# Kernel optimization log

Measured on AMD Instinct MI355X. Metric: run time of the kernel, lower is better.

Reference implementation:

```python
import jax, jax.numpy as jnp
import numpy as np

B, L, HID, TRANS = 16384, 512, 768, 128


def setup_inputs() -> dict:
    key = jax.random.key(0)
    ks = jax.random.split(key, 12)
    def lin(k, out_d, in_d):
        kw, kb = jax.random.split(k)
        s = 1.0 / np.sqrt(in_d)
        return (jax.random.uniform(kw, (out_d, in_d), jnp.float32, -s, s),
                jax.random.uniform(kb, (out_d,), jnp.float32, -s, s))
    W_text, b_text = lin(ks[0], TRANS, HID)
    W_label, b_label = lin(ks[1], TRANS, HID)
    W0, b0 = lin(ks[2], TRANS, 2 * TRANS)
    W1, b1 = lin(ks[3], TRANS, TRANS)
    W2, b2 = lin(ks[4], 1, TRANS)
    target = jax.random.randint(ks[5], (B, L), 0, 2, jnp.int32)
    # guarantee every sample has at least one positive label (torch.mean on empty would NaN)
    target = target.at[:, 0].set(1)
    return {
        "text_embed": jax.random.normal(ks[6], (B, HID), jnp.float32),
        "label_embed": jax.random.normal(ks[7], (L, HID), jnp.float32),
        "target": target,
        "perm": jax.random.permutation(ks[8], B).astype(jnp.int32),
        "W_text": W_text, "b_text": b_text,
        "W_label": W_label, "b_label": b_label,
        "W0": W0, "b0": b0, "W1": W1, "b1": b1, "W2": W2, "b2": b2,
    }


def _network(t, l, W_text, b_text, W_label, b_label, W0, b0, W1, b1, W2, b2):
    tt = t @ W_text.T + b_text            # [B, trans]
    ll = l @ W_label.T + b_label          # [B, trans]
    h = jnp.concatenate([tt, ll], axis=1)  # [B, 2*trans]
    h = jax.nn.relu(h @ W0.T + b0)
    h = jax.nn.relu(h @ W1.T + b1)
    return h @ W2.T + b2                  # [B, 1]


def reference(text_embed, label_embed, target, perm,
              W_text, b_text, W_label, b_label, W0, b0, W1, b1, W2, b2):
    # variable-length mean pooling of label embeddings selected by the multi-hot target
    mask = target.astype(text_embed.dtype)                 # [B, L]
    counts = jnp.maximum(mask.sum(axis=1, keepdims=True), 1.0)
    label_feature_y = (mask @ label_embed) / counts        # [B, hid]
    negative_text = text_embed[perm]                       # shuffled negatives
    params = (W_text, b_text, W_label, b_label, W0, b0, W1, b1, W2, b2)
    E_joint = -jnp.mean(jax.nn.softplus(-_network(text_embed, label_feature_y, *params)))
    E_marginal = jnp.mean(jax.nn.softplus(_network(negative_text, label_feature_y, *params)))
    return E_marginal - E_joint
```

## Files before the change

kernel.cpp:

```cpp
#include <hip/hip_runtime.h>
#include <math.h>

#define BATCH 16384
#define LBL   512
#define HID   768
#define TR    128

typedef unsigned long long u64;
typedef unsigned short ushort_t;
typedef __attribute__((ext_vector_type(8))) short short8;
typedef __attribute__((ext_vector_type(4))) float f32x4;

__device__ __forceinline__ ushort_t f2bf(float f){
  unsigned u = __builtin_bit_cast(unsigned, f);
  u += 0x7FFFu + ((u >> 16) & 1u);
  return (ushort_t)(u >> 16);
}
__device__ __forceinline__ float softplusf(float x){
  return fmaxf(x, 0.0f) + log1pf(expf(-fabsf(x)));
}
__device__ __forceinline__ void gload_lds16(const void* g, void* l){
  __builtin_amdgcn_global_load_lds((const __attribute__((address_space(1))) void*)g,
                                   (__attribute__((address_space(3))) void*)l, 16, 0, 0);
}

__global__ __launch_bounds__(256) void k1(
    const float* __restrict__ W0, const float* __restrict__ Wt, const float* __restrict__ Wl,
    const float* __restrict__ bt, const float* __restrict__ bl, const float* __restrict__ b0,
    const float* __restrict__ W1,
    ushort_t* __restrict__ Msw, ushort_t* __restrict__ Qsw, ushort_t* __restrict__ W1B,
    float* __restrict__ KV, float* __restrict__ out){
  __shared__ float sw[TR];
  int bi = blockIdx.x, t = threadIdx.x;
  if (bi < 256){
    int i = bi & 127;
    int isQ = bi >> 7;
    const float* src = isQ ? Wl : Wt;
    ushort_t* dst = isQ ? Qsw : Msw;
    if (t < TR) sw[t] = W0[(size_t)i*256 + isQ*128 + t];
    if (!isQ && t < 128) W1B[i*128 + t] = f2bf(W1[i*128 + t]);
    __syncthreads();
    int c = t;
    float a0 = 0.f, a1 = 0.f, a2 = 0.f;
    #pragma unroll 8
    for (int a = 0; a < 128; a++){
      float w = sw[a];
      const float* r = src + (size_t)a*HID;
      a0 = fmaf(w, r[c], a0);
      a1 = fmaf(w, r[c+256], a1);
      a2 = fmaf(w, r[c+512], a2);
    }
    int c7 = c & 7;
    dst[(((c      )>>3)<<10) + (i<<3) + c7] = f2bf(a0);
    dst[(((c + 256)>>3)<<10) + (i<<3) + c7] = f2bf(a1);
    dst[(((c + 512)>>3)<<10) + (i<<3) + c7] = f2bf(a2);
  } else {
    if (t < TR){
      float s = b0[t];
      const float* r = W0 + (size_t)t*256;
      for (int a = 0; a < 128; a++) s = fmaf(r[a], bt[a], s);
      for (int a = 0; a < 128; a++) s = fmaf(r[128+a], bl[a], s);
      KV[t] = s;
    }
    if (t == 0) out[0] = 0.f;
  }
}

__device__ __forceinline__ void gemm768_32(const float* ap, const ushort_t* Bsw,
                                           ushort_t* As_, ushort_t* Bs_,
                                           int tid, int wave, int m, int q,
                                           f32x4 acc[2][2]){
  float4 ra0 = *(const float4*)ap;
  float4 ra1 = *(const float4*)(ap + 4);
  {
    const char* gb = (const char*)Bsw;
    char* lb = (char*)Bs_;
    #pragma unroll
    for (int p = 0; p < 4; p++)
      gload_lds16(gb + p*4096 + tid*16, lb + p*4096 + tid*16);
  }
  #pragma unroll
  for (int rt = 0; rt < 2; rt++)
    #pragma unroll
    for (int ct = 0; ct < 2; ct++)
      acc[rt][ct] = (f32x4){0.f,0.f,0.f,0.f};

  for (int c = 0; c < 12; c++){
    int buf = c & 1;
    short8 av;
    av[0] = (short)f2bf(ra0.x); av[1] = (short)f2bf(ra0.y);
    av[2] = (short)f2bf(ra0.z); av[3] = (short)f2bf(ra0.w);
    av[4] = (short)f2bf(ra1.x); av[5] = (short)f2bf(ra1.y);
    av[6] = (short)f2bf(ra1.z); av[7] = (short)f2bf(ra1.w);
    *(short8*)(As_ + (size_t)(buf*32 + (tid >> 3))*80 + (tid & 7)*8) = av;
    __syncthreads();
    if (c < 11){
      ra0 = *(const float4*)(ap + (c+1)*64);
      ra1 = *(const float4*)(ap + (c+1)*64 + 4);
      const char* gb = (const char*)Bsw + (size_t)(c+1)*16384;
      char* lb = (char*)(Bs_ + (buf^1)*8192);
      #pragma unroll
      for (int p = 0; p < 4; p++)
        gload_lds16(gb + p*4096 + tid*16, lb + p*4096 + tid*16);
    }
    #pragma unroll
    for (int kcc = 0; kcc < 2; kcc++){
      short8 bfr[2];
      #pragma unroll
      for (int ct = 0; ct < 2; ct++)
        bfr[ct] = *(const short8*)(Bs_ + buf*8192 + (kcc*4 + q)*1024 + (wave*32 + ct*16 + m)*8);
      #pragma unroll
      for (int rt = 0; rt < 2; rt++){
        short8 a = *(const short8*)(As_ + (size_t)(buf*32 + rt*16 + m)*80 + kcc*32 + q*8);
        #pragma unroll
        for (int ct = 0; ct < 2; ct++)
          acc[rt][ct] = __builtin_amdgcn_mfma_f32_16x16x32_bf16(a, bfr[ct], acc[rt][ct], 0, 0, 0);
      }
    }
  }
}

__global__ __launch_bounds__(256) void k2(
    const float* __restrict__ labe, const ushort_t* __restrict__ Qsw,
    const int* __restrict__ tgt,
    ushort_t* __restrict__ Gt, u64* __restrict__ bits, float* __restrict__ inv){
  __shared__ __align__(16) char uni[43008];
  int bi = blockIdx.x, tid = threadIdx.x;
  int lane = tid & 63, wave = tid >> 6;
  int m = lane & 15, q = lane >> 4;
  ushort_t* Bs_ = (ushort_t*)uni;
  ushort_t* As_ = (ushort_t*)(uni + 32768);

  if (bi < 16){
    int l0 = bi * 32;
    int arow = tid >> 3, ak = (tid & 7) * 8;
    f32x4 accG[2][2];
    gemm768_32(labe + (size_t)(l0 + arow)*HID + ak, Qsw, As_, Bs_, tid, wave, m, q, accG);
    __syncthreads();
    ushort_t (*GTs)[40] = (ushort_t(*)[40])uni;
    #pragma unroll
    for (int rt = 0; rt < 2; rt++)
      #pragma unroll
      for (int ct = 0; ct < 2; ct++){
        int col = wave*32 + ct*16 + m;
        #pragma unroll
        for (int r = 0; r < 4; r++)
          GTs[col][rt*16 + q*4 + r] = f2bf(accG[rt][ct][r]);
      }
    __syncthreads();
    int gi = tid >> 1, half = tid & 1;
    ushort_t* dstp = Gt + (size_t)gi*LBL + l0 + half*16;
    *(short8*)(dstp)     = *(const short8*)&GTs[gi][half*16];
    *(short8*)(dstp + 8) = *(const short8*)&GTs[gi][half*16 + 8];
  } else {
    int b0r = (bi - 16)*32;
    #pragma unroll
    for (int rr = 0; rr < 8; rr++){
      int row = b0r + wave*8 + rr;
      const int* rp = tgt + (size_t)row*LBL;
      int v[8];
      #pragma unroll
      for (int c = 0; c < 8; c++) v[c] = rp[c*64 + lane];
      int cnt = 0;
      #pragma unroll
      for (int c = 0; c < 8; c++){
        u64 mm = __ballot(v[c] != 0);
        if (lane == 0){ bits[(size_t)row*8 + c] = mm; cnt += __popcll(mm); }
      }
      if (lane == 0) inv[row] = 1.0f / (float)(cnt < 1 ? 1 : cnt);
    }
  }
}

__global__ __launch_bounds__(256) void k3(const float* __restrict__ T, const ushort_t* __restrict__ Msw,
                                          const float* __restrict__ KV, const ushort_t* __restrict__ Gt,
                                          const u64* __restrict__ BITS_, const float* __restrict__ INV,
                                          const int* __restrict__ perm, const ushort_t* __restrict__ W1b,
                                          const float* __restrict__ b1, const float* __restrict__ W2,
                                          const float* __restrict__ b2, float* __restrict__ out){
  __shared__ __align__(16) char uni[51200];
  __shared__ __align__(16) u64 bitsS[32*10];
  __shared__ float invs[32];

  int tid = threadIdx.x;
  int lane = tid & 63, wave = tid >> 6;
  int m = lane & 15, q = lane >> 4;
  int r0 = blockIdx.x * 32;
  ushort_t* Bs_ = (ushort_t*)uni;
  ushort_t* As_ = (ushort_t*)(uni + 32768);

  if (tid < 128){
    int row = tid >> 2, seg = tid & 3;
    const int4* src = (const int4*)((const char*)BITS_ + (size_t)(r0+row)*64 + seg*16);
    *(int4*)((char*)bitsS + row*80 + seg*16) = *src;
  } else if (tid < 160){
    invs[tid & 31] = INV[r0 + (tid & 31)];
  }

  int ar = tid >> 3, ak = (tid & 7) * 8;
  const float* app = T + (size_t)(r0 + ar)*HID + ak;
  int pg = perm[r0 + ar];
  const float* apn = T + (size_t)pg*HID + ak;

  float4 pa0 = *(const float4*)(app);
  float4 pa1 = *(const float4*)(app + 4);
  float4 na0 = *(const float4*)(apn);
  float4 na1 = *(const float4*)(apn + 4);
  {
    const char* gb = (const char*)Msw;
    char* lb = (char*)Bs_;
    #pragma unroll
    for (int p = 0; p < 4; p++)
      gload_lds16(gb + p*4096 + tid*16, lb + p*4096 + tid*16);
  }
  f32x4 acc[4][2];
  #pragma unroll
  for (int rt = 0; rt < 4; rt++)
    #pragma unroll
    for (int ct = 0; ct < 2; ct++)
      acc[rt][ct] = (f32x4){0.f,0.f,0.f,0.f};

  for (int c = 0; c < 12; c++){
    int buf = c & 1;
    short8 pv, nv;
    pv[0]=(short)f2bf(pa0.x); pv[1]=(short)f2bf(pa0.y); pv[2]=(short)f2bf(pa0.z); pv[3]=(short)f2bf(pa0.w);
    pv[4]=(short)f2bf(pa1.x); pv[5]=(short)f2bf(pa1.y); pv[6]=(short)f2bf(pa1.z); pv[7]=(short)f2bf(pa1.w);
    nv[0]=(short)f2bf(na0.x); nv[1]=(short)f2bf(na0.y); nv[2]=(short)f2bf(na0.z); nv[3]=(short)f2bf(na0.w);
    nv[4]=(short)f2bf(na1.x); nv[5]=(short)f2bf(na1.y); nv[6]=(short)f2bf(na1.z); nv[7]=(short)f2bf(na1.w);
    *(short8*)(As_ + (size_t)(buf*64 + ar)*72 + ak)      = pv;
    *(short8*)(As_ + (size_t)(buf*64 + 32 + ar)*72 + ak) = nv;
    __syncthreads();
    if (c < 11){
      pa0 = *(const float4*)(app + (c+1)*64);
      pa1 = *(const float4*)(app + (c+1)*64 + 4);
      na0 = *(const float4*)(apn + (c+1)*64);
      na1 = *(const float4*)(apn + (c+1)*64 + 4);
      const char* gb = (const char*)Msw + (size_t)(c+1)*16384;
      char* lb = (char*)(Bs_ + (buf^1)*8192);
      #pragma unroll
      for (int p = 0; p < 4; p++)
        gload_lds16(gb + p*4096 + tid*16, lb + p*4096 + tid*16);
    }
    #pragma unroll
    for (int kcc = 0; kcc < 2; kcc++){
      short8 bfr[2];
      #pragma unroll
      for (int ct = 0; ct < 2; ct++)
        bfr[ct] = *(const short8*)(Bs_ + buf*8192 + (kcc*4 + q)*1024 + (wave*32 + ct*16 + m)*8);
      #pragma unroll
      for (int rt = 0; rt < 4; rt++){
        short8 a = *(const short8*)(As_ + (size_t)(buf*64 + rt*16 + m)*72 + kcc*32 + q*8);
        #pragma unroll
        for (int ct = 0; ct < 2; ct++)
          acc[rt][ct] = __builtin_amdgcn_mfma_f32_16x16x32_bf16(a, bfr[ct], acc[rt][ct], 0, 0, 0);
      }
    }
  }

  const unsigned char* bits_b = (const unsigned char*)bitsS;
  f32x4 accV[2][2] = {{{0,0,0,0},{0,0,0,0}},{{0,0,0,0},{0,0,0,0}}};
  const ushort_t* gp[2];
  #pragma unroll
  for (int ct = 0; ct < 2; ct++)
    gp[ct] = Gt + (size_t)(wave*32 + ct*16 + m)*LBL + q*8;
  short8 bcur[2], bnext[2];
  #pragma unroll
  for (int ct = 0; ct < 2; ct++) bcur[ct] = *(const short8*)(gp[ct]);
  for (int c = 0; c < 16; c++){
    if (c < 15){
      #pragma unroll
      for (int ct = 0; ct < 2; ct++) bnext[ct] = *(const short8*)(gp[ct] + (c+1)*32);
    }
    #pragma unroll
    for (int rt = 0; rt < 2; rt++){
      unsigned bb = bits_b[(rt*16 + m)*80 + c*4 + q];
      short8 a;
      #pragma unroll
      for (int j = 0; j < 8; j++) a[j] = (short)(((bb >> j) & 1u) ? 0x3F80 : 0);
      #pragma unroll
      for (int ct = 0; ct < 2; ct++)
        accV[rt][ct] = __builtin_amdgcn_mfma_f32_16x16x32_bf16(a, bcur[ct], accV[rt][ct], 0, 0, 0);
    }
    #pragma unroll
    for (int ct = 0; ct < 2; ct++) bcur[ct] = bnext[ct];
  }

  __syncthreads();
  ushort_t (*h0s)[136] = (ushort_t(*)[136])uni;
  float* sred = (float*)(uni + 17408);
  #pragma unroll
  for (int rt = 0; rt < 2; rt++)
    #pragma unroll
    for (int ct = 0; ct < 2; ct++){
      int col = wave*32 + ct*16 + m;
      float kv = KV[col];
      #pragma unroll
      for (int r = 0; r < 4; r++){
        int rowl = rt*16 + q*4 + r;
        float v = accV[rt][ct][r] * invs[rowl] + kv;
        h0s[rowl][col]      = f2bf(fmaxf(acc[rt][ct][r]   + v, 0.f));
        h0s[32 + rowl][col] = f2bf(fmaxf(acc[rt+2][ct][r] + v, 0.f));
      }
    }
  __syncthreads();

  float w2c[2], b1c[2];
  #pragma unroll
  for (int ct = 0; ct < 2; ct++){
    int col = wave*32 + ct*16 + m;
    w2c[ct] = W2[col];
    b1c[ct] = b1[col];
  }
  float b2v = b2[0];

  #pragma unroll
  for (int rt2 = 0; rt2 < 4; rt2++){
    f32x4 accH[2] = {{0,0,0,0},{0,0,0,0}};
    #pragma unroll
    for (int kc = 0; kc < 4; kc++){
      short8 a = *(const short8*)&h0s[rt2*16 + m][kc*32 + q*8];
      #pragma unroll
      for (int ct = 0; ct < 2; ct++){
        short8 b = *(const short8*)(W1b + (size_t)(wave*32 + ct*16 + m)*TR + kc*32 + q*8);
        accH[ct] = __builtin_amdgcn_mfma_f32_16x16x32_bf16(a, b, accH[ct], 0, 0, 0);
      }
    }
    #pragma unroll
    for (int r = 0; r < 4; r++){
      float sp = 0.f;
      #pragma unroll
      for (int ct = 0; ct < 2; ct++)
        sp = fmaf(w2c[ct], fmaxf(accH[ct][r] + b1c[ct], 0.f), sp);
      sred[((wave*4 + rt2)*16 + q*4 + r)*17 + m] = sp;
    }
  }
  __syncthreads();

  if (tid < 64){
    int rt2 = tid >> 4, row = tid & 15;
    float s = b2v;
    #pragma unroll
    for (int wx = 0; wx < 4; wx++)
      #pragma unroll
      for (int n = 0; n < 16; n++) s += sred[((wx*4 + rt2)*16 + row)*17 + n];
    float val = (rt2 < 2) ? softplusf(-s) : softplusf(s);
    #pragma unroll
    for (int off = 32; off > 0; off >>= 1) val += __shfl_down(val, off);
    if (tid == 0) atomicAdd(out, val * (1.0f / (float)BATCH));
  }
}

extern "C" void kernel_launch(void* const* d_in, const int* in_sizes, int n_in,
                              void* d_out, int out_size, void* d_ws, size_t ws_size,
                              hipStream_t stream){
  const float* text = (const float*)d_in[0];
  const float* labe = (const float*)d_in[1];
  const int*   tgt  = (const int*)  d_in[2];
  const int*   perm = (const int*)  d_in[3];
  const float* Wt   = (const float*)d_in[4];
  const float* bt   = (const float*)d_in[5];
  const float* Wl   = (const float*)d_in[6];
  const float* bl   = (const float*)d_in[7];
  const float* W0   = (const float*)d_in[8];
  const float* b0   = (const float*)d_in[9];
  const float* W1   = (const float*)d_in[10];
  const float* b1   = (const float*)d_in[11];
  const float* W2   = (const float*)d_in[12];
  const float* b2   = (const float*)d_in[13];

  char* wsb = (char*)d_ws;
  size_t off = 0;
  auto alloc = [&](size_t bytes){
    size_t r = off;
    off += (bytes + 255) & ~(size_t)255;
    return r;
  };
  ushort_t* MSW = (ushort_t*)(wsb + alloc((size_t)TR*HID*2));
  ushort_t* QSW = (ushort_t*)(wsb + alloc((size_t)TR*HID*2));
  ushort_t* GT  = (ushort_t*)(wsb + alloc((size_t)TR*LBL*2));
  ushort_t* W1B = (ushort_t*)(wsb + alloc((size_t)TR*TR*2));
  float*    KV  = (float*)   (wsb + alloc((size_t)TR*4));
  u64*      BITS= (u64*)     (wsb + alloc((size_t)BATCH*8*8));
  float*    INV = (float*)   (wsb + alloc((size_t)BATCH*4));
  float*    out = (float*)d_out;
  (void)ws_size; (void)in_sizes; (void)n_in; (void)out_size;

  k1<<<257, 256, 0, stream>>>(W0, Wt, Wl, bt, bl, b0, W1, MSW, QSW, W1B, KV, out);
  k2<<<528, 256, 0, stream>>>(labe, QSW, tgt, GT, BITS, INV);
  k3<<<512, 256, 0, stream>>>(text, MSW, KV, GT, BITS, INV, perm, W1B, b1, W2, b2, out);
}
```

Before: 171.9 us.

## Fuse target bitmask build into main kernel and widen it to 512 threads

Moves the ballot-based target bitmask and inverse-count computation out of k2 and into k3. Target rows are loaded into registers early and reduced mid-loop, which removes the global BITS/INV round trip and shrinks k2 to 16 blocks. k3 now runs 512 threads (8 waves), each wave owning 16 output columns instead of 32, and each thread loads one A row instead of both positive and negative rows. The risk is higher register pressure from holding 32 target ints per thread, and the final reduction loop over 128 columns is now serial per thread.

```diff
diff --git a/kernel.cpp b/kernel.cpp
--- a/kernel.cpp
+++ b/kernel.cpp
@@ -122,8 +122,7 @@
 
 __global__ __launch_bounds__(256) void k2(
     const float* __restrict__ labe, const ushort_t* __restrict__ Qsw,
-    const int* __restrict__ tgt,
-    ushort_t* __restrict__ Gt, u64* __restrict__ bits, float* __restrict__ inv){
+    ushort_t* __restrict__ Gt){
   __shared__ __align__(16) char uni[43008];
   int bi = blockIdx.x, tid = threadIdx.x;
   int lane = tid & 63, wave = tid >> 6;
@@ -131,50 +130,31 @@
   ushort_t* Bs_ = (ushort_t*)uni;
   ushort_t* As_ = (ushort_t*)(uni + 32768);
 
-  if (bi < 16){
-    int l0 = bi * 32;
-    int arow = tid >> 3, ak = (tid & 7) * 8;
-    f32x4 accG[2][2];
-    gemm768_32(labe + (size_t)(l0 + arow)*HID + ak, Qsw, As_, Bs_, tid, wave, m, q, accG);
-    __syncthreads();
-    ushort_t (*GTs)[40] = (ushort_t(*)[40])uni;
-    #pragma unroll
-    for (int rt = 0; rt < 2; rt++)
-      #pragma unroll
-      for (int ct = 0; ct < 2; ct++){
-        int col = wave*32 + ct*16 + m;
-        #pragma unroll
-        for (int r = 0; r < 4; r++)
-          GTs[col][rt*16 + q*4 + r] = f2bf(accG[rt][ct][r]);
-      }
-    __syncthreads();
-    int gi = tid >> 1, half = tid & 1;
-    ushort_t* dstp = Gt + (size_t)gi*LBL + l0 + half*16;
-    *(short8*)(dstp)     = *(const short8*)&GTs[gi][half*16];
-    *(short8*)(dstp + 8) = *(const short8*)&GTs[gi][half*16 + 8];
-  } else {
-    int b0r = (bi - 16)*32;
-    #pragma unroll
-    for (int rr = 0; rr < 8; rr++){
-      int row = b0r + wave*8 + rr;
-      const int* rp = tgt + (size_t)row*LBL;
-      int v[8];
-      #pragma unroll
-      for (int c = 0; c < 8; c++) v[c] = rp[c*64 + lane];
-      int cnt = 0;
-      #pragma unroll
-      for (int c = 0; c < 8; c++){
-        u64 mm = __ballot(v[c] != 0);
-        if (lane == 0){ bits[(size_t)row*8 + c] = mm; cnt += __popcll(mm); }
-      }
-      if (lane == 0) inv[row] = 1.0f / (float)(cnt < 1 ? 1 : cnt);
-    }
-  }
-}
-
-__global__ __launch_bounds__(256) void k3(const float* __restrict__ T, const ushort_t* __restrict__ Msw,
+  int l0 = bi * 32;
+  int arow = tid >> 3, ak = (tid & 7) * 8;
+  f32x4 accG[2][2];
+  gemm768_32(labe + (size_t)(l0 + arow)*HID + ak, Qsw, As_, Bs_, tid, wave, m, q, accG);
+  __syncthreads();
+  ushort_t (*GTs)[40] = (ushort_t(*)[40])uni;
+  #pragma unroll
+  for (int rt = 0; rt < 2; rt++)
+    #pragma unroll
+    for (int ct = 0; ct < 2; ct++){
+      int col = wave*32 + ct*16 + m;
+      #pragma unroll
+      for (int r = 0; r < 4; r++)
+        GTs[col][rt*16 + q*4 + r] = f2bf(accG[rt][ct][r]);
+    }
+  __syncthreads();
+  int gi = tid >> 1, half = tid & 1;
+  ushort_t* dstp = Gt + (size_t)gi*LBL + l0 + half*16;
+  *(short8*)(dstp)     = *(const short8*)&GTs[gi][half*16];
+  *(short8*)(dstp + 8) = *(const short8*)&GTs[gi][half*16 + 8];
+}
+
+__global__ __launch_bounds__(512, 4) void k3(const float* __restrict__ T, const ushort_t* __restrict__ Msw,
                                           const float* __restrict__ KV, const ushort_t* __restrict__ Gt,
-                                          const u64* __restrict__ BITS_, const float* __restrict__ INV,
+                                          const int* __restrict__ tgt,
                                           const int* __restrict__ perm, const ushort_t* __restrict__ W1b,
                                           const float* __restrict__ b1, const float* __restrict__ W2,
                                           const float* __restrict__ b2, float* __restrict__ out){
@@ -189,161 +169,129 @@
   ushort_t* Bs_ = (ushort_t*)uni;
   ushort_t* As_ = (ushort_t*)(uni + 32768);
 
-  if (tid < 128){
-    int row = tid >> 2, seg = tid & 3;
-    const int4* src = (const int4*)((const char*)BITS_ + (size_t)(r0+row)*64 + seg*16);
-    *(int4*)((char*)bitsS + row*80 + seg*16) = *src;
-  } else if (tid < 160){
-    invs[tid & 31] = INV[r0 + (tid & 31)];
-  }
-
   int ar = tid >> 3, ak = (tid & 7) * 8;
-  const float* app = T + (size_t)(r0 + ar)*HID + ak;
-  int pg = perm[r0 + ar];
-  const float* apn = T + (size_t)pg*HID + ak;
-
-  float4 pa0 = *(const float4*)(app);
-  float4 pa1 = *(const float4*)(app + 4);
-  float4 na0 = *(const float4*)(apn);
-  float4 na1 = *(const float4*)(apn + 4);
+  int arow = (ar < 32) ? (r0 + ar) : perm[r0 + ar - 32];
+  const float* app = T + (size_t)arow*HID + ak;
+
+  float4 a0 = *(const float4*)(app);
+  float4 a1 = *(const float4*)(app + 4);
   {
     const char* gb = (const char*)Msw;
     char* lb = (char*)Bs_;
-    #pragma unroll
-    for (int p = 0; p < 4; p++)
-      gload_lds16(gb + p*4096 + tid*16, lb + p*4096 + tid*16);
-  }
-  f32x4 acc[4][2];
-  #pragma unroll
-  for (int rt = 0; rt < 4; rt++)
-    #pragma unroll
-    for (int ct = 0; ct < 2; ct++)
-      acc[rt][ct] = (f32x4){0.f,0.f,0.f,0.f};
+    gload_lds16(gb + tid*16,        lb + tid*16);
+    gload_lds16(gb + 8192 + tid*16, lb + 8192 + tid*16);
+  }
+  int v[4][8];
+  #pragma unroll
+  for (int rr = 0; rr < 4; rr++){
+    const int* rp = tgt + (size_t)(r0 + wave*4 + rr)*LBL;
+    #pragma unroll
+    for (int cc = 0; cc < 8; cc++) v[rr][cc] = rp[cc*64 + lane];
+  }
+
+  f32x4 acc[4];
+  #pragma unroll
+  for (int rt = 0; rt < 4; rt++) acc[rt] = (f32x4){0.f,0.f,0.f,0.f};
 
   for (int c = 0; c < 12; c++){
     int buf = c & 1;
-    short8 pv, nv;
-    pv[0]=(short)f2bf(pa0.x); pv[1]=(short)f2bf(pa0.y); pv[2]=(short)f2bf(pa0.z); pv[3]=(short)f2bf(pa0.w);
-    pv[4]=(short)f2bf(pa1.x); pv[5]=(short)f2bf(pa1.y); pv[6]=(short)f2bf(pa1.z); pv[7]=(short)f2bf(pa1.w);
-    nv[0]=(short)f2bf(na0.x); nv[1]=(short)f2bf(na0.y); nv[2]=(short)f2bf(na0.z); nv[3]=(short)f2bf(na0.w);
-    nv[4]=(short)f2bf(na1.x); nv[5]=(short)f2bf(na1.y); nv[6]=(short)f2bf(na1.z); nv[7]=(short)f2bf(na1.w);
-    *(short8*)(As_ + (size_t)(buf*64 + ar)*72 + ak)      = pv;
-    *(short8*)(As_ + (size_t)(buf*64 + 32 + ar)*72 + ak) = nv;
+    short8 av;
+    av[0]=(short)f2bf(a0.x); av[1]=(short)f2bf(a0.y); av[2]=(short)f2bf(a0.z); av[3]=(short)f2bf(a0.w);
+    av[4]=(short)f2bf(a1.x); av[5]=(short)f2bf(a1.y); av[6]=(short)f2bf(a1.z); av[7]=(short)f2bf(a1.w);
+    *(short8*)(As_ + (size_t)(buf*64 + ar)*72 + ak) = av;
     __syncthreads();
+    if (c == 8){
+      #pragma unroll
+      for (int rr = 0; rr < 4; rr++){
+        int row = wave*4 + rr;
+        int cnt = 0;
+        #pragma unroll
+        for (int cc = 0; cc < 8; cc++){
+          u64 mm = __ballot(v[rr][cc] != 0);
+          if (lane == 0){ ((u64*)((char*)bitsS + row*80))[cc] = mm; cnt += __popcll(mm); }
+        }
+        if (lane == 0) invs[row] = 1.0f / (float)(cnt < 1 ? 1 : cnt);
+      }
+    }
     if (c < 11){
-      pa0 = *(const float4*)(app + (c+1)*64);
-      pa1 = *(const float4*)(app + (c+1)*64 + 4);
-      na0 = *(const float4*)(apn + (c+1)*64);
-      na1 = *(const float4*)(apn + (c+1)*64 + 4);
+      a0 = *(const float4*)(app + (c+1)*64);
+      a1 = *(const float4*)(app + (c+1)*64 + 4);
       const char* gb = (const char*)Msw + (size_t)(c+1)*16384;
       char* lb = (char*)(Bs_ + (buf^1)*8192);
-      #pragma unroll
-      for (int p = 0; p < 4; p++)
-        gload_lds16(gb + p*4096 + tid*16, lb + p*4096 + tid*16);
+      gload_lds16(gb + tid*16,        lb + tid*16);
+      gload_lds16(gb + 8192 + tid*16, lb + 8192 + tid*16);
     }
     #pragma unroll
     for (int kcc = 0; kcc < 2; kcc++){
-      short8 bfr[2];
-      #pragma unroll
-      for (int ct = 0; ct < 2; ct++)
-        bfr[ct] = *(const short8*)(Bs_ + buf*8192 + (kcc*4 + q)*1024 + (wave*32 + ct*16 + m)*8);
+      short8 bfr = *(const short8*)(Bs_ + buf*8192 + (kcc*4 + q)*1024 + (wave*16 + m)*8);
       #pragma unroll
       for (int rt = 0; rt < 4; rt++){
         short8 a = *(const short8*)(As_ + (size_t)(buf*64 + rt*16 + m)*72 + kcc*32 + q*8);
-        #pragma unroll
-        for (int ct = 0; ct < 2; ct++)
-          acc[rt][ct] = __builtin_amdgcn_mfma_f32_16x16x32_bf16(a, bfr[ct], acc[rt][ct], 0, 0, 0);
+        acc[rt] = __builtin_amdgcn_mfma_f32_16x16x32_bf16(a, bfr, acc[rt], 0, 0, 0);
       }
     }
   }
 
   const unsigned char* bits_b = (const unsigned char*)bitsS;
-  f32x4 accV[2][2] = {{{0,0,0,0},{0,0,0,0}},{{0,0,0,0},{0,0,0,0}}};
-  const ushort_t* gp[2];
-  #pragma unroll
-  for (int ct = 0; ct < 2; ct++)
-    gp[ct] = Gt + (size_t)(wave*32 + ct*16 + m)*LBL + q*8;
-  short8 bcur[2], bnext[2];
-  #pragma unroll
-  for (int ct = 0; ct < 2; ct++) bcur[ct] = *(const short8*)(gp[ct]);
+  f32x4 accV[2] = {{0,0,0,0},{0,0,0,0}};
+  const ushort_t* gp = Gt + (size_t)(wave*16 + m)*LBL + q*8;
+  short8 bv0 = *(const short8*)(gp);
+  short8 bv1 = *(const short8*)(gp + 32);
   for (int c = 0; c < 16; c++){
-    if (c < 15){
-      #pragma unroll
-      for (int ct = 0; ct < 2; ct++) bnext[ct] = *(const short8*)(gp[ct] + (c+1)*32);
-    }
+    short8 bn = bv1;
+    if (c < 14) bn = *(const short8*)(gp + (size_t)(c+2)*32);
     #pragma unroll
     for (int rt = 0; rt < 2; rt++){
       unsigned bb = bits_b[(rt*16 + m)*80 + c*4 + q];
       short8 a;
       #pragma unroll
       for (int j = 0; j < 8; j++) a[j] = (short)(((bb >> j) & 1u) ? 0x3F80 : 0);
-      #pragma unroll
-      for (int ct = 0; ct < 2; ct++)
-        accV[rt][ct] = __builtin_amdgcn_mfma_f32_16x16x32_bf16(a, bcur[ct], accV[rt][ct], 0, 0, 0);
-    }
-    #pragma unroll
-    for (int ct = 0; ct < 2; ct++) bcur[ct] = bnext[ct];
+      accV[rt] = __builtin_amdgcn_mfma_f32_16x16x32_bf16(a, bv0, accV[rt], 0, 0, 0);
+    }
+    bv0 = bv1; bv1 = bn;
   }
 
   __syncthreads();
   ushort_t (*h0s)[136] = (ushort_t(*)[136])uni;
   float* sred = (float*)(uni + 17408);
-  #pragma unroll
-  for (int rt = 0; rt < 2; rt++)
-    #pragma unroll
-    for (int ct = 0; ct < 2; ct++){
-      int col = wave*32 + ct*16 + m;
-      float kv = KV[col];
-      #pragma unroll
-      for (int r = 0; r < 4; r++){
-        int rowl = rt*16 + q*4 + r;
-        float v = accV[rt][ct][r] * invs[rowl] + kv;
-        h0s[rowl][col]      = f2bf(fmaxf(acc[rt][ct][r]   + v, 0.f));
-        h0s[32 + rowl][col] = f2bf(fmaxf(acc[rt+2][ct][r] + v, 0.f));
-      }
-    }
-  __syncthreads();
-
-  float w2c[2], b1c[2];
-  #pragma unroll
-  for (int ct = 0; ct < 2; ct++){
-    int col = wave*32 + ct*16 + m;
-    w2c[ct] = W2[col];
-    b1c[ct] = b1[col];
-  }
+  int col = wave*16 + m;
+  float kv = KV[col];
+  #pragma unroll
+  for (int rt = 0; rt < 2; rt++){
+    #pragma unroll
+    for (int r = 0; r < 4; r++){
+      int rowl = rt*16 + q*4 + r;
+      float vv = accV[rt][r] * invs[rowl] + kv;
+      h0s[rowl][col]      = f2bf(fmaxf(acc[rt][r]   + vv, 0.f));
+      h0s[32 + rowl][col] = f2bf(fmaxf(acc[rt+2][r] + vv, 0.f));
+    }
+  }
+  __syncthreads();
+
+  float w2c = W2[col], b1c = b1[col];
   float b2v = b2[0];
-
   #pragma unroll
   for (int rt2 = 0; rt2 < 4; rt2++){
-    f32x4 accH[2] = {{0,0,0,0},{0,0,0,0}};
+    f32x4 accH = {0,0,0,0};
     #pragma unroll
     for (int kc = 0; kc < 4; kc++){
       short8 a = *(const short8*)&h0s[rt2*16 + m][kc*32 + q*8];
-      #pragma unroll
-      for (int ct = 0; ct < 2; ct++){
-        short8 b = *(const short8*)(W1b + (size_t)(wave*32 + ct*16 + m)*TR + kc*32 + q*8);
-        accH[ct] = __builtin_amdgcn_mfma_f32_16x16x32_bf16(a, b, accH[ct], 0, 0, 0);
-      }
+      short8 b = *(const short8*)(W1b + (size_t)col*TR + kc*32 + q*8);
+      accH = __builtin_amdgcn_mfma_f32_16x16x32_bf16(a, b, accH, 0, 0, 0);
     }
     #pragma unroll
     for (int r = 0; r < 4; r++){
-      float sp = 0.f;
-      #pragma unroll
-      for (int ct = 0; ct < 2; ct++)
-        sp = fmaf(w2c[ct], fmaxf(accH[ct][r] + b1c[ct], 0.f), sp);
-      sred[((wave*4 + rt2)*16 + q*4 + r)*17 + m] = sp;
+      float sp = w2c * fmaxf(accH[r] + b1c, 0.f);
+      sred[(size_t)(rt2*16 + q*4 + r)*129 + col] = sp;
     }
   }
   __syncthreads();
 
   if (tid < 64){
-    int rt2 = tid >> 4, row = tid & 15;
     float s = b2v;
     #pragma unroll
-    for (int wx = 0; wx < 4; wx++)
-      #pragma unroll
-      for (int n = 0; n < 16; n++) s += sred[((wx*4 + rt2)*16 + row)*17 + n];
-    float val = (rt2 < 2) ? softplusf(-s) : softplusf(s);
+    for (int n = 0; n < 128; n++) s += sred[(size_t)tid*129 + n];
+    float val = (tid < 32) ? softplusf(-s) : softplusf(s);
     #pragma unroll
     for (int off = 32; off > 0; off >>= 1) val += __shfl_down(val, off);
     if (tid == 0) atomicAdd(out, val * (1.0f / (float)BATCH));
@@ -380,12 +328,10 @@
   ushort_t* GT  = (ushort_t*)(wsb + alloc((size_t)TR*LBL*2));
   ushort_t* W1B = (ushort_t*)(wsb + alloc((size_t)TR*TR*2));
   float*    KV  = (float*)   (wsb + alloc((size_t)TR*4));
-  u64*      BITS= (u64*)     (wsb + alloc((size_t)BATCH*8*8));
-  float*    INV = (float*)   (wsb + alloc((size_t)BATCH*4));
   float*    out = (float*)d_out;
   (void)ws_size; (void)in_sizes; (void)n_in; (void)out_size;
 
   k1<<<257, 256, 0, stream>>>(W0, Wt, Wl, bt, bl, b0, W1, MSW, QSW, W1B, KV, out);
-  k2<<<528, 256, 0, stream>>>(labe, QSW, tgt, GT, BITS, INV);
-  k3<<<512, 256, 0, stream>>>(text, MSW, KV, GT, BITS, INV, perm, W1B, b1, W2, b2, out);
-}
+  k2<<<16, 256, 0, stream>>>(labe, QSW, GT);
+  k3<<<512, 512, 0, stream>>>(text, MSW, KV, GT, tgt, perm, W1B, b1, W2, b2, out);
+}
```

After: 166.5 us. 1.03x faster.
